# Performance work log

Measured on AMD Instinct MI355X. Metric: run time of the kernel, lower is better.

Reference implementation:

```python
import jax, jax.numpy as jnp
import numpy as np

B, L, C = 256, 16384, 4
DMICE_P = 0.1
IGNORE = 3  # padding class, also ignore_index for CE


def setup_inputs() -> dict:
    key = jax.random.key(0)
    k1, k2, k3 = jax.random.split(key, 3)
    pred = jax.random.normal(k1, (B, C, L), dtype=jnp.float32)
    # real labels in {0,1,2}; tail after a random length is padded with 3
    base = jax.random.randint(k2, (B, L), 0, 3, dtype=jnp.int32)
    lengths = jax.random.randint(k3, (B,), L // 2, L, dtype=jnp.int32)
    valid = jnp.arange(L, dtype=jnp.int32)[None, :] < lengths[:, None]
    labels = jnp.where(valid, base, IGNORE)
    return {"pred": pred, "labels": labels}


def reference(pred, labels):
    # pred: [B, C=4, L] logits; labels: [B, L] int in {0,1,2,3}, 3 = pad/ignore
    b, c, l = pred.shape
    f32 = pred.dtype

    # --- CrossEntropyLoss(ignore_index=3), mean over valid tokens ---
    valid = (labels != IGNORE)
    logp = jax.nn.log_softmax(pred, axis=1)                         # [B,4,L]
    picked = jnp.take_along_axis(logp, labels[:, None, :], axis=1)[:, 0, :]  # [B,L]
    ce = -(picked * valid.astype(f32)).sum() / valid.sum().astype(f32)

    # --- per-sample ragged prefix length j (first label==3, else L-1) ---
    is_pad = (labels == IGNORE)
    has_pad = jnp.any(is_pad, axis=1)
    j = jnp.where(has_pad, jnp.argmax(is_pad, axis=1), l - 1)        # [B]
    mask = (jnp.arange(l)[None, :] < j[:, None]).astype(f32)         # [B,L]

    # --- DMI: mat = onehot(labels)^T @ softmax(pred[:, :3]) / j ---
    probs = jax.nn.softmax(pred[:, :3, :], axis=1)                   # [B,3,L]
    onehot = jax.nn.one_hot(labels, 3, dtype=f32) * mask[..., None]  # [B,L,3]
    mat = jnp.einsum('blc,bdl->bcd', onehot, probs) / j[:, None, None].astype(f32)  # [B,3,3]
    det = jnp.linalg.det(mat)                                        # [B]
    dmi = jnp.where(det < 0,
                    jnp.log(jnp.abs(det) + 1e-3),
                    -jnp.log(jnp.abs(det) + 1e-3))
    loss = DMICE_P * (dmi.sum() / b) + ce
    return loss
```

## Files before the change

kernel.cpp:

```cpp
#include <hip/hip_runtime.h>
#include <math.h>

constexpr int B_ = 256;
constexpr int L_ = 16384;
constexpr int C_ = 4;
constexpr int CHUNKS = 16;
constexpr int CHUNK = L_ / CHUNKS;
constexpr int THREADS = 256;
constexpr int NVAL = 11;
constexpr int PSTRIDE = 12;
constexpr int NBLK = B_ * CHUNKS;

__global__ __launch_bounds__(THREADS) void dmice_partial(
    const float* __restrict__ pred, const int* __restrict__ labels,
    float* __restrict__ partial) {
  const int blk = blockIdx.x;
  const int b = blk >> 4;
  const int ch = blk & (CHUNKS - 1);

  const float* p0 = pred + (size_t)b * (C_ * L_) + (size_t)ch * CHUNK;
  const float* p1 = p0 + L_;
  const float* p2 = p0 + 2 * L_;
  const float* p3 = p0 + 3 * L_;
  const int* lb = labels + (size_t)b * L_ + (size_t)ch * CHUNK;
  const int t = threadIdx.x;
  const int idx = t * 4;

  const int4 l = *(const int4*)(lb + idx);
  const float4 x0 = *(const float4*)(p0 + idx);
  const float4 x1 = *(const float4*)(p1 + idx);
  const float4 x2 = *(const float4*)(p2 + idx);
  const float4 x3 = *(const float4*)(p3 + idx);

  float ce = 0.f, cnt = 0.f;
  float m00 = 0.f, m01 = 0.f, m02 = 0.f;
  float m10 = 0.f, m11 = 0.f, m12 = 0.f;
  float m20 = 0.f, m21 = 0.f, m22 = 0.f;

  auto proc = [&](float v0, float v1, float v2, float v3, int lab) {
    float mx = fmaxf(fmaxf(v0, v1), fmaxf(v2, v3));
    float e0 = __expf(v0 - mx);
    float e1 = __expf(v1 - mx);
    float e2 = __expf(v2 - mx);
    float e3 = __expf(v3 - mx);
    float s3 = e0 + e1 + e2;
    float s4 = s3 + e3;
    if (lab != 3) {
      float xl = (lab == 0) ? v0 : ((lab == 1) ? v1 : v2);
      ce += (mx + __logf(s4)) - xl;
      cnt += 1.f;
      float inv = 1.f / s3;
      float r0 = (lab == 0) ? inv : 0.f;
      float r1 = (lab == 1) ? inv : 0.f;
      float r2 = (lab == 2) ? inv : 0.f;
      m00 = fmaf(e0, r0, m00); m01 = fmaf(e1, r0, m01); m02 = fmaf(e2, r0, m02);
      m10 = fmaf(e0, r1, m10); m11 = fmaf(e1, r1, m11); m12 = fmaf(e2, r1, m12);
      m20 = fmaf(e0, r2, m20); m21 = fmaf(e1, r2, m21); m22 = fmaf(e2, r2, m22);
    }
  };

  proc(x0.x, x1.x, x2.x, x3.x, l.x);
  proc(x0.y, x1.y, x2.y, x3.y, l.y);
  proc(x0.z, x1.z, x2.z, x3.z, l.z);
  proc(x0.w, x1.w, x2.w, x3.w, l.w);

  float vals[NVAL] = {ce, cnt, m00, m01, m02, m10, m11, m12, m20, m21, m22};
#pragma unroll
  for (int off = 32; off > 0; off >>= 1) {
#pragma unroll
    for (int k = 0; k < NVAL; ++k) vals[k] += __shfl_down(vals[k], off, 64);
  }
  __shared__ float red[THREADS / 64][NVAL];
  const int wave = t >> 6, lane = t & 63;
  if (lane == 0) {
#pragma unroll
    for (int k = 0; k < NVAL; ++k) red[wave][k] = vals[k];
  }
  __syncthreads();
  if (t == 0) {
    float s[NVAL];
#pragma unroll
    for (int k = 0; k < NVAL; ++k)
      s[k] = red[0][k] + red[1][k] + red[2][k] + red[3][k];
    float* pp = partial + (size_t)blk * PSTRIDE;
    *(float4*)(pp + 0) = make_float4(s[0], s[1], s[2], s[3]);
    *(float4*)(pp + 4) = make_float4(s[4], s[5], s[6], s[7]);
    *(float4*)(pp + 8) = make_float4(s[8], s[9], s[10], 0.f);
  }
}

__global__ __launch_bounds__(THREADS) void dmice_final(
    const float* __restrict__ partial, float* __restrict__ out) {
  const int b = threadIdx.x;
  float v[NVAL];
#pragma unroll
  for (int k = 0; k < NVAL; ++k) v[k] = 0.f;
  for (int c = 0; c < CHUNKS; ++c) {
    const float* p = partial + (size_t)(b * CHUNKS + c) * PSTRIDE;
#pragma unroll
    for (int k = 0; k < NVAL; ++k) v[k] += p[k];
  }
  float ce = v[0], cnt = v[1];
  float inv = 1.f / cnt;
  float a00 = v[2] * inv, a01 = v[3] * inv, a02 = v[4] * inv;
  float a10 = v[5] * inv, a11 = v[6] * inv, a12 = v[7] * inv;
  float a20 = v[8] * inv, a21 = v[9] * inv, a22 = v[10] * inv;
  float det = a00 * (a11 * a22 - a12 * a21)
            - a01 * (a10 * a22 - a12 * a20)
            + a02 * (a10 * a21 - a11 * a20);
  float lg = __logf(fabsf(det) + 1e-3f);
  float dmi = (det < 0.f) ? lg : -lg;

  float r[3] = {dmi, ce, cnt};
#pragma unroll
  for (int off = 32; off > 0; off >>= 1) {
#pragma unroll
    for (int k = 0; k < 3; ++k) r[k] += __shfl_down(r[k], off, 64);
  }
  __shared__ float red[THREADS / 64][3];
  const int wave = b >> 6, lane = b & 63;
  if (lane == 0) {
#pragma unroll
    for (int k = 0; k < 3; ++k) red[wave][k] = r[k];
  }
  __syncthreads();
  if (b == 0) {
    float dmi_s = red[0][0] + red[1][0] + red[2][0] + red[3][0];
    float ce_s  = red[0][1] + red[1][1] + red[2][1] + red[3][1];
    float cnt_s = red[0][2] + red[1][2] + red[2][2] + red[3][2];
    out[0] = 0.1f * (dmi_s * (1.f / (float)B_)) + ce_s / cnt_s;
  }
}

extern "C" void kernel_launch(void* const* d_in, const int* in_sizes, int n_in,
                              void* d_out, int out_size, void* d_ws, size_t ws_size,
                              hipStream_t stream) {
  const float* pred = (const float*)d_in[0];
  const int* labels = (const int*)d_in[1];
  float* out = (float*)d_out;
  float* partial = (float*)d_ws;

  dmice_partial<<<NBLK, THREADS, 0, stream>>>(pred, labels, partial);
  dmice_final<<<1, THREADS, 0, stream>>>(partial, out);
}
```

Measured before the change: 112.6 us.

## Process one batch row per 1024-thread block and compute determinant in-block

Replaces the 4096-block chunked partial reduction with 256 blocks of 1024 threads, each covering a full row with a 4-iteration unrolled loop. The per-row 3x3 determinant and DMI term are now computed in the first kernel, so the final kernel only reduces three values per row. This removes the partial-buffer writes and reads and the 16-way per-row accumulation in the final kernel. In exchange, only 256 blocks are launched, which may underfill the GPU's compute units and lower the number of memory requests in flight for this bandwidth-bound read.

```diff
diff --git a/kernel.cpp b/kernel.cpp
--- a/kernel.cpp
+++ b/kernel.cpp
@@ -4,33 +4,20 @@
 constexpr int B_ = 256;
 constexpr int L_ = 16384;
 constexpr int C_ = 4;
-constexpr int CHUNKS = 16;
-constexpr int CHUNK = L_ / CHUNKS;
-constexpr int THREADS = 256;
+constexpr int THREADS = 1024;
 constexpr int NVAL = 11;
-constexpr int PSTRIDE = 12;
-constexpr int NBLK = B_ * CHUNKS;
+constexpr int NWAVE = THREADS / 64;
 
-__global__ __launch_bounds__(THREADS) void dmice_partial(
+__global__ __launch_bounds__(THREADS) void dmice_row(
     const float* __restrict__ pred, const int* __restrict__ labels,
-    float* __restrict__ partial) {
-  const int blk = blockIdx.x;
-  const int b = blk >> 4;
-  const int ch = blk & (CHUNKS - 1);
-
-  const float* p0 = pred + (size_t)b * (C_ * L_) + (size_t)ch * CHUNK;
+    float* __restrict__ rowout) {
+  const int b = blockIdx.x;
+  const float* p0 = pred + (size_t)b * (C_ * L_);
   const float* p1 = p0 + L_;
   const float* p2 = p0 + 2 * L_;
   const float* p3 = p0 + 3 * L_;
-  const int* lb = labels + (size_t)b * L_ + (size_t)ch * CHUNK;
+  const int* lb = labels + (size_t)b * L_;
   const int t = threadIdx.x;
-  const int idx = t * 4;
-
-  const int4 l = *(const int4*)(lb + idx);
-  const float4 x0 = *(const float4*)(p0 + idx);
-  const float4 x1 = *(const float4*)(p1 + idx);
-  const float4 x2 = *(const float4*)(p2 + idx);
-  const float4 x3 = *(const float4*)(p3 + idx);
 
   float ce = 0.f, cnt = 0.f;
   float m00 = 0.f, m01 = 0.f, m02 = 0.f;
@@ -59,10 +46,20 @@
     }
   };
 
-  proc(x0.x, x1.x, x2.x, x3.x, l.x);
-  proc(x0.y, x1.y, x2.y, x3.y, l.y);
-  proc(x0.z, x1.z, x2.z, x3.z, l.z);
-  proc(x0.w, x1.w, x2.w, x3.w, l.w);
+  constexpr int ITERS = L_ / (THREADS * 4);
+#pragma unroll
+  for (int it = 0; it < ITERS; ++it) {
+    const int idx = (it * THREADS + t) * 4;
+    const int4 l = *(const int4*)(lb + idx);
+    const float4 x0 = *(const float4*)(p0 + idx);
+    const float4 x1 = *(const float4*)(p1 + idx);
+    const float4 x2 = *(const float4*)(p2 + idx);
+    const float4 x3 = *(const float4*)(p3 + idx);
+    proc(x0.x, x1.x, x2.x, x3.x, l.x);
+    proc(x0.y, x1.y, x2.y, x3.y, l.y);
+    proc(x0.z, x1.z, x2.z, x3.z, l.z);
+    proc(x0.w, x1.w, x2.w, x3.w, l.w);
+  }
 
   float vals[NVAL] = {ce, cnt, m00, m01, m02, m10, m11, m12, m20, m21, m22};
 #pragma unroll
@@ -70,7 +67,7 @@
 #pragma unroll
     for (int k = 0; k < NVAL; ++k) vals[k] += __shfl_down(vals[k], off, 64);
   }
-  __shared__ float red[THREADS / 64][NVAL];
+  __shared__ float red[NWAVE][NVAL];
   const int wave = t >> 6, lane = t & 63;
   if (lane == 0) {
 #pragma unroll
@@ -80,44 +77,37 @@
   if (t == 0) {
     float s[NVAL];
 #pragma unroll
-    for (int k = 0; k < NVAL; ++k)
-      s[k] = red[0][k] + red[1][k] + red[2][k] + red[3][k];
-    float* pp = partial + (size_t)blk * PSTRIDE;
-    *(float4*)(pp + 0) = make_float4(s[0], s[1], s[2], s[3]);
-    *(float4*)(pp + 4) = make_float4(s[4], s[5], s[6], s[7]);
-    *(float4*)(pp + 8) = make_float4(s[8], s[9], s[10], 0.f);
+    for (int k = 0; k < NVAL; ++k) {
+      float acc = 0.f;
+#pragma unroll
+      for (int w = 0; w < NWAVE; ++w) acc += red[w][k];
+      s[k] = acc;
+    }
+    float cs = s[1];
+    float inv = 1.f / cs;
+    float a00 = s[2] * inv, a01 = s[3] * inv, a02 = s[4] * inv;
+    float a10 = s[5] * inv, a11 = s[6] * inv, a12 = s[7] * inv;
+    float a20 = s[8] * inv, a21 = s[9] * inv, a22 = s[10] * inv;
+    float det = a00 * (a11 * a22 - a12 * a21)
+              - a01 * (a10 * a22 - a12 * a20)
+              + a02 * (a10 * a21 - a11 * a20);
+    float lg = __logf(fabsf(det) + 1e-3f);
+    float dmi = (det < 0.f) ? lg : -lg;
+    *(float4*)(rowout + (size_t)b * 4) = make_float4(dmi, s[0], cs, 0.f);
   }
 }
 
-__global__ __launch_bounds__(THREADS) void dmice_final(
-    const float* __restrict__ partial, float* __restrict__ out) {
+__global__ __launch_bounds__(256) void dmice_final(
+    const float* __restrict__ rowout, float* __restrict__ out) {
   const int b = threadIdx.x;
-  float v[NVAL];
-#pragma unroll
-  for (int k = 0; k < NVAL; ++k) v[k] = 0.f;
-  for (int c = 0; c < CHUNKS; ++c) {
-    const float* p = partial + (size_t)(b * CHUNKS + c) * PSTRIDE;
-#pragma unroll
-    for (int k = 0; k < NVAL; ++k) v[k] += p[k];
-  }
-  float ce = v[0], cnt = v[1];
-  float inv = 1.f / cnt;
-  float a00 = v[2] * inv, a01 = v[3] * inv, a02 = v[4] * inv;
-  float a10 = v[5] * inv, a11 = v[6] * inv, a12 = v[7] * inv;
-  float a20 = v[8] * inv, a21 = v[9] * inv, a22 = v[10] * inv;
-  float det = a00 * (a11 * a22 - a12 * a21)
-            - a01 * (a10 * a22 - a12 * a20)
-            + a02 * (a10 * a21 - a11 * a20);
-  float lg = __logf(fabsf(det) + 1e-3f);
-  float dmi = (det < 0.f) ? lg : -lg;
-
-  float r[3] = {dmi, ce, cnt};
+  const float4 v = *(const float4*)(rowout + (size_t)b * 4);
+  float r[3] = {v.x, v.y, v.z};
 #pragma unroll
   for (int off = 32; off > 0; off >>= 1) {
 #pragma unroll
     for (int k = 0; k < 3; ++k) r[k] += __shfl_down(r[k], off, 64);
   }
-  __shared__ float red[THREADS / 64][3];
+  __shared__ float red[4][3];
   const int wave = b >> 6, lane = b & 63;
   if (lane == 0) {
 #pragma unroll
@@ -138,8 +128,8 @@
   const float* pred = (const float*)d_in[0];
   const int* labels = (const int*)d_in[1];
   float* out = (float*)d_out;
-  float* partial = (float*)d_ws;
+  float* rowout = (float*)d_ws;
 
-  dmice_partial<<<NBLK, THREADS, 0, stream>>>(pred, labels, partial);
-  dmice_final<<<1, THREADS, 0, stream>>>(partial, out);
+  dmice_row<<<B_, THREADS, 0, stream>>>(pred, labels, rowout);
+  dmice_final<<<1, 256, 0, stream>>>(rowout, out);
 }
```

Result: faster. 105.0 us (-6.8%).
